# Performance work log

Hardware: AMD Instinct MI355X
Metric: run time of the kernel (lower is better)

The kernel has to match this reference:

```python
import jax, jax.numpy as jnp
import numpy as np

DIM = 4096
HEADS = 32
HEAD_DIM = 128
FFN_INNER = 4 * DIM  # GEGLU inner
EPS = 1e-6


def _mk(key, shape, scale=0.02):
    return jax.random.normal(key, shape, dtype=jnp.float32) * scale


def setup_inputs() -> dict:
    key = jax.random.key(0)
    ks = jax.random.split(key, 20)
    inp = {
        "video": jax.random.normal(ks[0], (1, 4096, DIM), dtype=jnp.float32),
        "text": jax.random.normal(ks[1], (1, 256, DIM), dtype=jnp.float32),
        # self-attention projections
        "wq": _mk(ks[2], (DIM, DIM)),
        "wk": _mk(ks[3], (DIM, DIM)),
        "wv": _mk(ks[4], (DIM, DIM)),
        "wo": _mk(ks[5], (DIM, DIM)),
        "q_norm_w": jnp.ones((DIM,), jnp.float32),
        "k_norm_w": jnp.ones((DIM,), jnp.float32),
        # cross-attention projections (q from video, k/v from text)
        "cwq": _mk(ks[6], (DIM, DIM)),
        "cwk": _mk(ks[7], (DIM, DIM)),
        "cwv": _mk(ks[8], (DIM, DIM)),
        "cwo": _mk(ks[9], (DIM, DIM)),
        "cq_norm_w": jnp.ones((DIM,), jnp.float32),
        "ck_norm_w": jnp.ones((DIM,), jnp.float32),
        # GEGLU FFN: proj -> (value, gate) -> value * gelu(gate) -> down
        "w_ff_proj": _mk(ks[10], (DIM, 2 * FFN_INNER)),
        "w_ff_down": _mk(ks[11], (FFN_INNER, DIM)),
    }
    return inp


def rmsnorm(x, w, eps=EPS):
    # RMSNorm over full hidden dim in fp32 (matches DistributedRMSNorm global math)
    x32 = x.astype(jnp.float32)
    rms = jax.lax.rsqrt(jnp.mean(x32 * x32, axis=-1, keepdims=True) + eps)
    return (x32 * rms) * w


def split_heads(x):  # [b,s,dim] -> [b,h,s,hd]
    b, s, _ = x.shape
    return x.reshape(b, s, HEADS, HEAD_DIM).transpose(0, 2, 1, 3)


def merge_heads(x):  # [b,h,s,hd] -> [b,s,dim]
    b, h, s, hd = x.shape
    return x.transpose(0, 2, 1, 3).reshape(b, s, h * hd)


def bmm_sdpa(q, k, v):
    # BMM + softmax fallback (explicit score matrix, as on Neuron)
    scale = 1.0 / np.sqrt(HEAD_DIM)
    scores = jnp.einsum("bhqd,bhkd->bhqk", q, k) * scale
    probs = jax.nn.softmax(scores, axis=-1)
    return jnp.einsum("bhqk,bhkd->bhqd", probs, v)


def attention(x_q, x_kv, wq, wk, wv, wo, qn, kn):
    q = rmsnorm(x_q @ wq, qn)
    k = rmsnorm(x_kv @ wk, kn)
    v = x_kv @ wv
    out = bmm_sdpa(split_heads(q), split_heads(k), split_heads(v))
    return merge_heads(out) @ wo


def geglu_ffn(x, w_proj, w_down):
    h = x @ w_proj
    val, gate = jnp.split(h, 2, axis=-1)
    return (val * jax.nn.gelu(gate)) @ w_down


def reference(video, text, wq, wk, wv, wo, q_norm_w, k_norm_w,
              cwq, cwk, cwv, cwo, cq_norm_w, ck_norm_w,
              w_ff_proj, w_ff_down):
    # video self-attention block slice
    h = video + attention(video, video, wq, wk, wv, wo, q_norm_w, k_norm_w)
    # text cross-attention
    h = h + attention(h, text, cwq, cwk, cwv, cwo, cq_norm_w, ck_norm_w)
    # GEGLU feed-forward
    h = h + geglu_ffn(h, w_ff_proj, w_ff_down)
    return h
```

## Files before the change

### kernel.cpp

```cpp
#include <hip/hip_runtime.h>
#include <cstdint>
#include <cstddef>

typedef __bf16 bf16;
typedef __bf16 bf16x8 __attribute__((ext_vector_type(8)));
typedef __bf16 bf16x4 __attribute__((ext_vector_type(4)));
typedef float f32x4 __attribute__((ext_vector_type(4)));

static constexpr int D = 4096;
static constexpr int S = 4096;
static constexpr int T = 256;
static constexpr int H = 32;
static constexpr int F = 16384;

__device__ __forceinline__ void gload16(const void* g, void* l) {
  __builtin_amdgcn_global_load_lds((const __attribute__((address_space(1))) void*)g,
                                   (__attribute__((address_space(3))) void*)l, 16, 0, 0);
}

#define MFMA16(a, b, c) __builtin_amdgcn_mfma_f32_16x16x32_bf16((a), (b), (c), 0, 0, 0)

__global__ __launch_bounds__(256) void k_cvt(const float* __restrict__ in, bf16* __restrict__ out, int n) {
  int i = (blockIdx.x * 256 + threadIdx.x) * 4;
  if (i >= n) return;
  float4 v = *(const float4*)(in + i);
  bf16x4 o = { (bf16)v.x, (bf16)v.y, (bf16)v.z, (bf16)v.w };
  *(bf16x4*)(out + i) = o;
}

__global__ __launch_bounds__(256) void k_tc(const float* __restrict__ in, bf16* __restrict__ out,
                                            int R, int C, int ldin) {
  __shared__ float tile[32][33];
  int c0 = blockIdx.x * 32, r0 = blockIdx.y * 32;
  int x = threadIdx.x, y = threadIdx.y;
  #pragma unroll
  for (int yy = y; yy < 32; yy += 8)
    tile[yy][x] = in[(size_t)(r0 + yy) * ldin + c0 + x];
  __syncthreads();
  #pragma unroll
  for (int yy = y; yy < 32; yy += 8)
    out[(size_t)(c0 + yy) * R + r0 + x] = (bf16)tile[x][yy];
}

__global__ __launch_bounds__(256) void k_tb(const bf16* __restrict__ in, bf16* __restrict__ out, int R, int C) {
  __shared__ bf16 tile[32][33];
  int c0 = blockIdx.x * 32, r0 = blockIdx.y * 32;
  int x = threadIdx.x, y = threadIdx.y;
  #pragma unroll
  for (int yy = y; yy < 32; yy += 8)
    tile[yy][x] = in[(size_t)(r0 + yy) * C + c0 + x];
  __syncthreads();
  #pragma unroll
  for (int yy = y; yy < 32; yy += 8)
    out[(size_t)(c0 + yy) * R + r0 + x] = tile[x][yy];
}

__global__ __launch_bounds__(256) void k_rms(const float* __restrict__ in, const float* __restrict__ w,
                                             bf16* __restrict__ out) {
  const int row = blockIdx.x, t = threadIdx.x;
  const float* x = in + (size_t)row * 4096;
  float4 v[4];
  float ss = 0.f;
  #pragma unroll
  for (int i = 0; i < 4; i++) {
    v[i] = *(const float4*)(x + t * 4 + i * 1024);
    ss += v[i].x * v[i].x + v[i].y * v[i].y + v[i].z * v[i].z + v[i].w * v[i].w;
  }
  #pragma unroll
  for (int off = 1; off < 64; off <<= 1) ss += __shfl_xor(ss, off, 64);
  __shared__ float red[4];
  if ((t & 63) == 0) red[t >> 6] = ss;
  __syncthreads();
  float rms = rsqrtf((red[0] + red[1] + red[2] + red[3]) * (1.f / 4096.f) + 1e-6f);
  #pragma unroll
  for (int i = 0; i < 4; i++) {
    const float4 wv = *(const float4*)(w + t * 4 + i * 1024);
    bf16x4 ov = { (bf16)(v[i].x * rms * wv.x), (bf16)(v[i].y * rms * wv.y),
                  (bf16)(v[i].z * rms * wv.z), (bf16)(v[i].w * rms * wv.w) };
    *(bf16x4*)(out + (size_t)row * 4096 + t * 4 + i * 1024) = ov;
  }
}

__device__ __forceinline__ void xcd_map(int orig, int XGM, int BYG, int BXG, int& by, int& bx) {
  const int xcd = orig & 7, oidx = orig >> 3;
  by = (xcd % XGM) * BYG + oidx % BYG;
  bx = (xcd / XGM) * BXG + oidx / BYG;
}

template <int MODE>
__global__ __launch_bounds__(512, 2) void k_gemm2(const bf16* __restrict__ A, const bf16* __restrict__ BT,
                                                  float* __restrict__ Cf, bf16* __restrict__ Cb,
                                                  const float* __restrict__ res,
                                                  int M, int N, int K, int XGM, int BYG, int BXG) {
  __shared__ bf16 LA[2][2][256 * 32];
  __shared__ bf16 LB[2][2][256 * 32];
  int by, bx;
  xcd_map(blockIdx.x, XGM, BYG, BXG, by, bx);
  const size_t m0 = (size_t)by * 256, n0 = (size_t)bx * 256;
  const int t = threadIdx.x;
  const int w = t >> 6, lane = t & 63;
  const int wm = w >> 2, wn = w & 3;
  const int g = lane >> 4, r15 = lane & 15;
  const int nt = K >> 6;
  const int sr0 = t >> 2, ss0 = t & 3;
  const int sr1 = (t + 512) >> 2, ss1 = (t + 512) & 3;
  const int sc0 = ((ss0 ^ ((sr0 >> 1) & 3)) << 3);
  const int sc1 = ((ss1 ^ ((sr1 >> 1) & 3)) << 3);
  f32x4 acc[8][4] = {};

  auto stA = [&](int db, int kh, int st) {
    const bf16* src = A + m0 * K + (size_t)st * 64 + kh * 32;
    gload16(src + (size_t)sr0 * K + sc0, &LA[db][kh][t * 8]);
    gload16(src + (size_t)sr1 * K + sc1, &LA[db][kh][(t + 512) * 8]);
  };
  auto stB = [&](int db, int kh, int st) {
    const bf16* src = BT + n0 * K + (size_t)st * 64 + kh * 32;
    gload16(src + (size_t)sr0 * K + sc0, &LB[db][kh][t * 8]);
    gload16(src + (size_t)sr1 * K + sc1, &LB[db][kh][(t + 512) * 8]);
  };

  stA(0, 0, 0); stB(0, 0, 0); stA(0, 1, 0); stB(0, 1, 0);
  stA(1, 0, 1); stB(1, 0, 1); stA(1, 1, 1);
  asm volatile("s_waitcnt vmcnt(6)" ::: "memory");
  __builtin_amdgcn_s_barrier();

  const int arow = wm * 128;

#define GEMM_TILE(DD, TC)                                                                     \
  {                                                                                           \
    const int t1 = ((TC) + 1 < nt) ? (TC) + 1 : nt - 1;                                       \
    const int t2 = ((TC) + 2 < nt) ? (TC) + 2 : nt - 1;                                       \
    bf16x8 af[8], b0, b1;                                                                     \
                                                                     \
    stB((DD) ^ 1, 1, t1);                                                                     \
    _Pragma("unroll")                                                                         \
    for (int mf = 0; mf < 8; ++mf) {                                                          \
      const int rr = arow + mf * 16 + r15;                                                    \
      af[mf] = *(const bf16x8*)&LA[DD][0][rr * 32 + ((g ^ ((rr >> 1) & 3)) << 3)];            \
    }                                                                                         \
    {                                                                                         \
      const int rb0 = wn * 64 + r15, rb1 = wn * 64 + 16 + r15;                                \
      b0 = *(const bf16x8*)&LB[DD][0][rb0 * 32 + ((g ^ ((rb0 >> 1) & 3)) << 3)];              \
      b1 = *(const bf16x8*)&LB[DD][0][rb1 * 32 + ((g ^ ((rb1 >> 1) & 3)) << 3)];              \
    }                                                                                         \
    __builtin_amdgcn_s_barrier();                                                             \
    __builtin_amdgcn_s_setprio(1);                                                            \
    _Pragma("unroll")                                                                         \
    for (int mf = 0; mf < 8; ++mf) {                                                          \
      acc[mf][0] = MFMA16(af[mf], b0, acc[mf][0]);                                            \
      acc[mf][1] = MFMA16(af[mf], b1, acc[mf][1]);                                            \
    }                                                                                         \
    __builtin_amdgcn_s_setprio(0);                                                            \
                                                                     \
    stA(DD, 0, t2);                                                                           \
    {                                                                                         \
      const int rb0 = wn * 64 + 32 + r15, rb1 = wn * 64 + 48 + r15;                           \
      b0 = *(const bf16x8*)&LB[DD][0][rb0 * 32 + ((g ^ ((rb0 >> 1) & 3)) << 3)];              \
      b1 = *(const bf16x8*)&LB[DD][0][rb1 * 32 + ((g ^ ((rb1 >> 1) & 3)) << 3)];              \
    }                                                                                         \
    __builtin_amdgcn_s_barrier();                                                             \
    __builtin_amdgcn_s_setprio(1);                                                            \
    _Pragma("unroll")                                                                         \
    for (int mf = 0; mf < 8; ++mf) {                                                          \
      acc[mf][2] = MFMA16(af[mf], b0, acc[mf][2]);                                            \
      acc[mf][3] = MFMA16(af[mf], b1, acc[mf][3]);                                            \
    }                                                                                         \
    __builtin_amdgcn_s_setprio(0);                                                            \
                                                                     \
    stB(DD, 0, t2);                                                                           \
    _Pragma("unroll")                                                                         \
    for (int mf = 0; mf < 8; ++mf) {                                                          \
      const int rr = arow + mf * 16 + r15;                                                    \
      af[mf] = *(const bf16x8*)&LA[DD][1][rr * 32 + ((g ^ ((rr >> 1) & 3)) << 3)];            \
    }                                                                                         \
    {                                                                                         \
      const int rb0 = wn * 64 + r15, rb1 = wn * 64 + 16 + r15;                                \
      b0 = *(const bf16x8*)&LB[DD][1][rb0 * 32 + ((g ^ ((rb0 >> 1) & 3)) << 3)];              \
      b1 = *(const bf16x8*)&LB[DD][1][rb1 * 32 + ((g ^ ((rb1 >> 1) & 3)) << 3)];              \
    }                                                                                         \
    __builtin_amdgcn_s_barrier();                                                             \
    __builtin_amdgcn_s_setprio(1);                                                            \
    _Pragma("unroll")                                                                         \
    for (int mf = 0; mf < 8; ++mf) {                                                          \
      acc[mf][0] = MFMA16(af[mf], b0, acc[mf][0]);                                            \
      acc[mf][1] = MFMA16(af[mf], b1, acc[mf][1]);                                            \
    }                                                                                         \
    __builtin_amdgcn_s_setprio(0);                                                            \
                                                                     \
    stA(DD, 1, t2);                                                                           \
    {                                                                                         \
      const int rb0 = wn * 64 + 32 + r15, rb1 = wn * 64 + 48 + r15;                           \
      b0 = *(const bf16x8*)&LB[DD][1][rb0 * 32 + ((g ^ ((rb0 >> 1) & 3)) << 3)];              \
      b1 = *(const bf16x8*)&LB[DD][1][rb1 * 32 + ((g ^ ((rb1 >> 1) & 3)) << 3)];              \
    }                                                                                         \
    asm volatile("s_waitcnt vmcnt(6)" ::: "memory");                                          \
    __builtin_amdgcn_s_barrier();                                                             \
    __builtin_amdgcn_s_setprio(1);                                                            \
    _Pragma("unroll")                                                                         \
    for (int mf = 0; mf < 8; ++mf) {                                                          \
      acc[mf][2] = MFMA16(af[mf], b0, acc[mf][2]);                                            \
      acc[mf][3] = MFMA16(af[mf], b1, acc[mf][3]);                                            \
    }                                                                                         \
    __builtin_amdgcn_s_setprio(0);                                                            \
  }

  for (int tt = 0; tt < nt; tt += 2) {
    GEMM_TILE(0, tt);
    GEMM_TILE(1, tt + 1);
  }
#undef GEMM_TILE

  #pragma unroll
  for (int mf = 0; mf < 8; ++mf)
    #pragma unroll
    for (int nf = 0; nf < 4; ++nf) {
      const size_t col = n0 + wn * 64 + nf * 16 + r15;
      #pragma unroll
      for (int rr = 0; rr < 4; ++rr) {
        const size_t row = m0 + wm * 128 + mf * 16 + g * 4 + rr;
        const size_t idx = row * (size_t)N + col;
        const float v = acc[mf][nf][rr];
        if (MODE == 0) Cf[idx] = v;
        else if (MODE == 1) Cb[idx] = (bf16)v;
        else Cf[idx] = v + res[idx];
      }
    }
}

__global__ __launch_bounds__(512, 2) void k_geglu2(const bf16* __restrict__ A, const bf16* __restrict__ BT,
                                                   bf16* __restrict__ G, int N, int K,
                                                   int XGM, int BYG, int BXG) {
  __shared__ bf16 LA[2][2][256 * 32];
  __shared__ bf16 LBv[2][2][128 * 32];
  __shared__ bf16 LBg[2][2][128 * 32];
  int by, bx;
  xcd_map(blockIdx.x, XGM, BYG, BXG, by, bx);
  const size_t m0 = (size_t)by * 256, n0 = (size_t)bx * 128;
  const int t = threadIdx.x;
  const int w = t >> 6, lane = t & 63;
  const int wm = w >> 2, wn = w & 3;
  const int g = lane >> 4, r15 = lane & 15;
  const int nt = K >> 6;
  const int sr0 = t >> 2, ss0 = t & 3;
  const int sr1 = (t + 512) >> 2, ss1 = (t + 512) & 3;
  const int sc0 = ((ss0 ^ ((sr0 >> 1) & 3)) << 3);
  const int sc1 = ((ss1 ^ ((sr1 >> 1) & 3)) << 3);
  f32x4 av[8][2] = {}, ag[8][2] = {};

  auto stA = [&](int db, int kh, int st) {
    const bf16* src = A + m0 * K + (size_t)st * 64 + kh * 32;
    gload16(src + (size_t)sr0 * K + sc0, &LA[db][kh][t * 8]);
    gload16(src + (size_t)sr1 * K + sc1, &LA[db][kh][(t + 512) * 8]);
  };
  auto stBv = [&](int db, int kh, int st) {
    const bf16* src = BT + n0 * K + (size_t)st * 64 + kh * 32;
    gload16(src + (size_t)sr0 * K + sc0, &LBv[db][kh][t * 8]);
  };
  auto stBg = [&](int db, int kh, int st) {
    const bf16* src = BT + ((size_t)N + n0) * K + (size_t)st * 64 + kh * 32;
    gload16(src + (size_t)sr0 * K + sc0, &LBg[db][kh][t * 8]);
  };

  stA(0, 0, 0); stBv(0, 0, 0); stBg(0, 0, 0); stA(0, 1, 0); stBv(0, 1, 0); stBg(0, 1, 0);
  stA(1, 0, 1); stBv(1, 0, 1); stBg(1, 0, 1); stA(1, 1, 1);
  asm volatile("s_waitcnt vmcnt(6)" ::: "memory");
  __builtin_amdgcn_s_barrier();

  const int arow = wm * 128;

#define GEGLU_TILE(DD, TC)                                                                    \
  {                                                                                           \
    const int t1 = ((TC) + 1 < nt) ? (TC) + 1 : nt - 1;                                       \
    const int t2 = ((TC) + 2 < nt) ? (TC) + 2 : nt - 1;                                       \
    bf16x8 af[8], b0, b1;                                                                     \
                                                                      \
    stBv((DD) ^ 1, 1, t1); stBg((DD) ^ 1, 1, t1);                                             \
    _Pragma("unroll")                                                                         \
    for (int mf = 0; mf < 8; ++mf) {                                                          \
      const int rr = arow + mf * 16 + r15;                                                    \
      af[mf] = *(const bf16x8*)&LA[DD][0][rr * 32 + ((g ^ ((rr >> 1) & 3)) << 3)];            \
    }                                                                                         \
    {                                                                                         \
      const int rb0 = wn * 32 + r15, rb1 = wn * 32 + 16 + r15;                                \
      b0 = *(const bf16x8*)&LBv[DD][0][rb0 * 32 + ((g ^ ((rb0 >> 1) & 3)) << 3)];             \
      b1 = *(const bf16x8*)&LBv[DD][0][rb1 * 32 + ((g ^ ((rb1 >> 1) & 3)) << 3)];             \
    }                                                                                         \
    __builtin_amdgcn_s_barrier();                                                             \
    __builtin_amdgcn_s_setprio(1);                                                            \
    _Pragma("unroll")                                                                         \
    for (int mf = 0; mf < 8; ++mf) {                                                          \
      av[mf][0] = MFMA16(af[mf], b0, av[mf][0]);                                              \
      av[mf][1] = MFMA16(af[mf], b1, av[mf][1]);                                              \
    }                                                                                         \
    __builtin_amdgcn_s_setprio(0);                                                            \
                                                                     \
    stA(DD, 0, t2);                                                                           \
    {                                                                                         \
      const int rb0 = wn * 32 + r15, rb1 = wn * 32 + 16 + r15;                                \
      b0 = *(const bf16x8*)&LBg[DD][0][rb0 * 32 + ((g ^ ((rb0 >> 1) & 3)) << 3)];             \
      b1 = *(const bf16x8*)&LBg[DD][0][rb1 * 32 + ((g ^ ((rb1 >> 1) & 3)) << 3)];             \
    }                                                                                         \
    __builtin_amdgcn_s_barrier();                                                             \
    __builtin_amdgcn_s_setprio(1);                                                            \
    _Pragma("unroll")                                                                         \
    for (int mf = 0; mf < 8; ++mf) {                                                          \
      ag[mf][0] = MFMA16(af[mf], b0, ag[mf][0]);                                              \
      ag[mf][1] = MFMA16(af[mf], b1, ag[mf][1]);                                              \
    }                                                                                         \
    __builtin_amdgcn_s_setprio(0);                                                            \
                                                                      \
    stBv(DD, 0, t2); stBg(DD, 0, t2);                                                         \
    _Pragma("unroll")                                                                         \
    for (int mf = 0; mf < 8; ++mf) {                                                          \
      const int rr = arow + mf * 16 + r15;                                                    \
      af[mf] = *(const bf16x8*)&LA[DD][1][rr * 32 + ((g ^ ((rr >> 1) & 3)) << 3)];            \
    }                                                                                         \
    {                                                                                         \
      const int rb0 = wn * 32 + r15, rb1 = wn * 32 + 16 + r15;                                \
      b0 = *(const bf16x8*)&LBv[DD][1][rb0 * 32 + ((g ^ ((rb0 >> 1) & 3)) << 3)];             \
      b1 = *(const bf16x8*)&LBv[DD][1][rb1 * 32 + ((g ^ ((rb1 >> 1) & 3)) << 3)];             \
    }                                                                                         \
    __builtin_amdgcn_s_barrier();                                                             \
    __builtin_amdgcn_s_setprio(1);                                                            \
    _Pragma("unroll")                                                                         \
    for (int mf = 0; mf < 8; ++mf) {                                                          \
      av[mf][0] = MFMA16(af[mf], b0, av[mf][0]);                                              \
      av[mf][1] = MFMA16(af[mf], b1, av[mf][1]);                                              \
    }                                                                                         \
    __builtin_amdgcn_s_setprio(0);                                                            \
                                                                     \
    stA(DD, 1, t2);                                                                           \
    {                                                                                         \
      const int rb0 = wn * 32 + r15, rb1 = wn * 32 + 16 + r15;                                \
      b0 = *(const bf16x8*)&LBg[DD][1][rb0 * 32 + ((g ^ ((rb0 >> 1) & 3)) << 3)];             \
      b1 = *(const bf16x8*)&LBg[DD][1][rb1 * 32 + ((g ^ ((rb1 >> 1) & 3)) << 3)];             \
    }                                                                                         \
    asm volatile("s_waitcnt vmcnt(6)" ::: "memory");                                          \
    __builtin_amdgcn_s_barrier();                                                             \
    __builtin_amdgcn_s_setprio(1);                                                            \
    _Pragma("unroll")                                                                         \
    for (int mf = 0; mf < 8; ++mf) {                                                          \
      ag[mf][0] = MFMA16(af[mf], b0, ag[mf][0]);                                              \
      ag[mf][1] = MFMA16(af[mf], b1, ag[mf][1]);                                              \
    }                                                                                         \
    __builtin_amdgcn_s_setprio(0);                                                            \
  }

  for (int tt = 0; tt < nt; tt += 2) {
    GEGLU_TILE(0, tt);
    GEGLU_TILE(1, tt + 1);
  }
#undef GEGLU_TILE

  #pragma unroll
  for (int mf = 0; mf < 8; ++mf)
    #pragma unroll
    for (int nf = 0; nf < 2; ++nf) {
      const size_t col = n0 + wn * 32 + nf * 16 + r15;
      #pragma unroll
      for (int rr = 0; rr < 4; ++rr) {
        const size_t row = m0 + wm * 128 + mf * 16 + g * 4 + rr;
        const float val = av[mf][nf][rr], gt = ag[mf][nf][rr];
        const float z = 1.595769122f * gt + 0.0713548162f * gt * gt * gt;
        const float gel = gt / (1.f + __expf(-z));
        G[row * (size_t)N + col] = (bf16)(val * gel);
      }
    }
}

template <int MODE>
__global__ __launch_bounds__(256) void k_gemm128(const bf16* __restrict__ A, const bf16* __restrict__ BT,
                                                 float* __restrict__ Cf, bf16* __restrict__ Cb,
                                                 int M, int N, int K) {
  __shared__ bf16 As[128 * 32];
  __shared__ bf16 Bs[128 * 32];
  const int t = threadIdx.x;
  const int lane = t & 63, w = t >> 6;
  const int wr = w >> 1, wc = w & 1;
  const int g = lane >> 4, r15 = lane & 15;
  const size_t m0 = (size_t)blockIdx.y * 128, n0 = (size_t)blockIdx.x * 128;
  f32x4 acc[4][4] = {};
  const int c0 = t, c1 = t + 256;
  const int ar0 = c0 >> 2, as0 = c0 & 3, ar1 = c1 >> 2, as1 = c1 & 3;
  const bf16* Ab = A + m0 * K;
  const bf16* Bb = BT + n0 * K;
  for (int k0 = 0; k0 < K; k0 += 32) {
    __syncthreads();
    gload16(Ab + (size_t)ar0 * K + k0 + ((as0 ^ (ar0 & 3)) << 3), &As[c0 * 8]);
    gload16(Ab + (size_t)ar1 * K + k0 + ((as1 ^ (ar1 & 3)) << 3), &As[c1 * 8]);
    gload16(Bb + (size_t)ar0 * K + k0 + ((as0 ^ (ar0 & 3)) << 3), &Bs[c0 * 8]);
    gload16(Bb + (size_t)ar1 * K + k0 + ((as1 ^ (ar1 & 3)) << 3), &Bs[c1 * 8]);
    __syncthreads();
    bf16x8 af[4], bfr[4];
    #pragma unroll
    for (int mi = 0; mi < 4; mi++) {
      int row = wr * 64 + mi * 16 + r15;
      af[mi] = *(const bf16x8*)&As[row * 32 + ((g ^ (row & 3)) << 3)];
    }
    #pragma unroll
    for (int ni = 0; ni < 4; ni++) {
      int row = wc * 64 + ni * 16 + r15;
      bfr[ni] = *(const bf16x8*)&Bs[row * 32 + ((g ^ (row & 3)) << 3)];
    }
    #pragma unroll
    for (int mi = 0; mi < 4; mi++)
      #pragma unroll
      for (int ni = 0; ni < 4; ni++)
        acc[mi][ni] = MFMA16(af[mi], bfr[ni], acc[mi][ni]);
  }
  #pragma unroll
  for (int mi = 0; mi < 4; mi++)
    #pragma unroll
    for (int ni = 0; ni < 4; ni++) {
      size_t col = n0 + wc * 64 + ni * 16 + r15;
      #pragma unroll
      for (int rr = 0; rr < 4; rr++) {
        size_t row = m0 + wr * 64 + mi * 16 + g * 4 + rr;
        size_t idx = row * (size_t)N + col;
        float v = acc[mi][ni][rr];
        if (MODE == 0) Cf[idx] = v;
        else Cb[idx] = (bf16)v;
      }
    }
}

__global__ __launch_bounds__(256) void k_attn(const bf16* __restrict__ Q, const bf16* __restrict__ Kb,
                                              const bf16* __restrict__ VT, bf16* __restrict__ O,
                                              int Skv) {
  __shared__ bf16 Kt[32 * 128];
  __shared__ bf16 Vt[128 * 32];
  __shared__ bf16 Pt[4][16 * 32];
  const int h = blockIdx.y;
  const int t = threadIdx.x, w = t >> 6, lane = t & 63;
  const int g = lane >> 4, r15 = lane & 15;
  const int q0 = blockIdx.x * 64 + w * 16;
  bf16x8 qf[4];
  #pragma unroll
  for (int c = 0; c < 4; c++)
    qf[c] = *(const bf16x8*)(Q + (size_t)(q0 + r15) * D + h * 128 + c * 32 + g * 8);
  f32x4 o[8] = {};
  float m_[4] = { -1e30f, -1e30f, -1e30f, -1e30f };
  float l_[4] = { 0.f, 0.f, 0.f, 0.f };
  const float scale = 0.08838834764831845f;
  for (int kt = 0; kt < Skv; kt += 32) {
    __syncthreads();
    #pragma unroll
    for (int cc = 0; cc < 2; cc++) {
      int c = t + cc * 256;
      int kr = c >> 4, ks = c & 15;
      gload16(Kb + (size_t)(kt + kr) * D + h * 128 + ((ks ^ (kr & 15)) << 3), &Kt[c * 8]);
      int vr = c >> 2, vs = c & 3;
      gload16(VT + (size_t)(h * 128 + vr) * Skv + kt + ((vs ^ (vr & 3)) << 3), &Vt[c * 8]);
    }
    __syncthreads();
    f32x4 s0 = {}, s1 = {};
    #pragma unroll
    for (int c = 0; c < 4; c++) {
      int row0 = r15, row1 = 16 + r15;
      bf16x8 kf0 = *(const bf16x8*)&Kt[row0 * 128 + (((4 * c + g) ^ (row0 & 15)) << 3)];
      bf16x8 kf1 = *(const bf16x8*)&Kt[row1 * 128 + (((4 * c + g) ^ (row1 & 15)) << 3)];
      s0 = MFMA16(qf[c], kf0, s0);
      s1 = MFMA16(qf[c], kf1, s1);
    }
    float al[4];
    #pragma unroll
    for (int rr = 0; rr < 4; rr++) {
      float v0 = s0[rr] * scale, v1 = s1[rr] * scale;
      float mx = fmaxf(v0, v1);
      #pragma unroll
      for (int off = 1; off < 16; off <<= 1) mx = fmaxf(mx, __shfl_xor(mx, off, 16));
      float mn = fmaxf(m_[rr], mx);
      al[rr] = __expf(m_[rr] - mn);
      float p0 = __expf(v0 - mn), p1 = __expf(v1 - mn);
      float sm = p0 + p1;
      #pragma unroll
      for (int off = 1; off < 16; off <<= 1) sm += __shfl_xor(sm, off, 16);
      l_[rr] = l_[rr] * al[rr] + sm;
      m_[rr] = mn;
      int prow = g * 4 + rr;
      int sl0 = r15 >> 3, sl1 = 2 + (r15 >> 3);
      Pt[w][prow * 32 + ((sl0 ^ (prow & 3)) << 3) + (r15 & 7)] = (bf16)p0;
      Pt[w][prow * 32 + ((sl1 ^ (prow & 3)) << 3) + (r15 & 7)] = (bf16)p1;
    }
    #pragma unroll
    for (int d = 0; d < 8; d++)
      #pragma unroll
      for (int rr = 0; rr < 4; rr++) o[d][rr] *= al[rr];
    bf16x8 pa = *(const bf16x8*)&Pt[w][r15 * 32 + ((g ^ (r15 & 3)) << 3)];
    #pragma unroll
    for (int d = 0; d < 8; d++) {
      int vrow = d * 16 + r15;
      bf16x8 vbf = *(const bf16x8*)&Vt[vrow * 32 + ((g ^ (vrow & 3)) << 3)];
      o[d] = MFMA16(pa, vbf, o[d]);
    }
  }
  #pragma unroll
  for (int rr = 0; rr < 4; rr++) {
    float inv = 1.f / l_[rr];
    #pragma unroll
    for (int d = 0; d < 8; d++)
      O[(size_t)(q0 + g * 4 + rr) * D + h * 128 + d * 16 + r15] = (bf16)(o[d][rr] * inv);
  }
}

extern "C" void kernel_launch(void* const* d_in, const int* in_sizes, int n_in,
                              void* d_out, int out_size, void* d_ws, size_t ws_size,
                              hipStream_t stream) {
  (void)in_sizes; (void)n_in; (void)out_size; (void)ws_size;
  const float* video = (const float*)d_in[0];
  const float* text  = (const float*)d_in[1];
  const float* wq    = (const float*)d_in[2];
  const float* wk    = (const float*)d_in[3];
  const float* wv    = (const float*)d_in[4];
  const float* wo    = (const float*)d_in[5];
  const float* qnw   = (const float*)d_in[6];
  const float* knw   = (const float*)d_in[7];
  const float* cwq   = (const float*)d_in[8];
  const float* cwk   = (const float*)d_in[9];
  const float* cwv   = (const float*)d_in[10];
  const float* cwo   = (const float*)d_in[11];
  const float* cqnw  = (const float*)d_in[12];
  const float* cknw  = (const float*)d_in[13];
  const float* ffp   = (const float*)d_in[14];
  const float* ffd   = (const float*)d_in[15];
  float* out = (float*)d_out;

  char* slab = (char*)d_ws;
  const size_t MB = 1024 * 1024;
  bf16*  wbuf  = (bf16*)slab;
  bf16*  vb    = (bf16*)(slab + 64 * MB);
  bf16*  vt    = (bf16*)(slab + 96 * MB);
  float* pre   = (float*)(slab + 128 * MB);
  bf16*  Hval  = (bf16*)(slab + 268 * MB);
  char* p = slab + 402 * MB;
  auto take = [&](size_t bytes) { char* r = p; p += (bytes + 255) & ~(size_t)255; return r; };
  bf16* xb   = (bf16*)take((size_t)S * D * 2);
  bf16* qb   = (bf16*)take((size_t)S * D * 2);
  bf16* kb   = (bf16*)take((size_t)S * D * 2);
  bf16* ab   = (bf16*)take((size_t)S * D * 2);
  float* h1  = (float*)take((size_t)S * D * 4);
  bf16* tbuf = (bf16*)take((size_t)T * D * 2);
  bf16* ckb  = (bf16*)take((size_t)T * D * 2);
  bf16* cvb  = (bf16*)take((size_t)T * D * 2);
  bf16* cvt_ = (bf16*)take((size_t)T * D * 2);
  float* h2  = out;

  dim3 b256(256), b512(512), btc(32, 8);
  const int GRID_DD = 256, GRID_GG = 2048;

  k_cvt<<<(S * D) / 1024, b256, 0, stream>>>(video, xb, S * D);
  k_tc<<<dim3(D / 32, D / 32), btc, 0, stream>>>(wq, wbuf, D, D, D);
  k_gemm2<0><<<GRID_DD, b512, 0, stream>>>(xb, wbuf, pre, nullptr, nullptr, S, D, D, 2, 8, 4);
  k_rms<<<S, b256, 0, stream>>>(pre, qnw, qb);
  k_tc<<<dim3(D / 32, D / 32), btc, 0, stream>>>(wk, wbuf, D, D, D);
  k_gemm2<0><<<GRID_DD, b512, 0, stream>>>(xb, wbuf, pre, nullptr, nullptr, S, D, D, 2, 8, 4);
  k_rms<<<S, b256, 0, stream>>>(pre, knw, kb);
  k_tc<<<dim3(D / 32, D / 32), btc, 0, stream>>>(wv, wbuf, D, D, D);
  k_gemm2<1><<<GRID_DD, b512, 0, stream>>>(xb, wbuf, nullptr, vb, nullptr, S, D, D, 2, 8, 4);
  k_tb<<<dim3(D / 32, S / 32), btc, 0, stream>>>(vb, vt, S, D);
  k_attn<<<dim3(S / 64, H), b256, 0, stream>>>(qb, kb, vt, ab, S);
  k_tc<<<dim3(D / 32, D / 32), btc, 0, stream>>>(wo, wbuf, D, D, D);
  k_gemm2<2><<<GRID_DD, b512, 0, stream>>>(ab, wbuf, h1, nullptr, video, S, D, D, 2, 8, 4);

  k_cvt<<<(S * D) / 1024, b256, 0, stream>>>(h1, xb, S * D);
  k_tc<<<dim3(D / 32, D / 32), btc, 0, stream>>>(cwq, wbuf, D, D, D);
  k_gemm2<0><<<GRID_DD, b512, 0, stream>>>(xb, wbuf, pre, nullptr, nullptr, S, D, D, 2, 8, 4);
  k_rms<<<S, b256, 0, stream>>>(pre, cqnw, qb);
  k_cvt<<<(T * D) / 1024, b256, 0, stream>>>(text, tbuf, T * D);
  k_tc<<<dim3(D / 32, D / 32), btc, 0, stream>>>(cwk, wbuf, D, D, D);
  k_gemm128<0><<<dim3(D / 128, T / 128), b256, 0, stream>>>(tbuf, wbuf, pre, nullptr, T, D, D);
  k_rms<<<T, b256, 0, stream>>>(pre, cknw, ckb);
  k_tc<<<dim3(D / 32, D / 32), btc, 0, stream>>>(cwv, wbuf, D, D, D);
  k_gemm128<1><<<dim3(D / 128, T / 128), b256, 0, stream>>>(tbuf, wbuf, nullptr, cvb, T, D, D);
  k_tb<<<dim3(D / 32, T / 32), btc, 0, stream>>>(cvb, cvt_, T, D);
  k_attn<<<dim3(S / 64, H), b256, 0, stream>>>(qb, ckb, cvt_, ab, T);
  k_tc<<<dim3(D / 32, D / 32), btc, 0, stream>>>(cwo, wbuf, D, D, D);
  k_gemm2<2><<<GRID_DD, b512, 0, stream>>>(ab, wbuf, h2, nullptr, h1, S, D, D, 2, 8, 4);

  k_cvt<<<(S * D) / 1024, b256, 0, stream>>>(h2, xb, S * D);
  k_tc<<<dim3((2 * F) / 32, D / 32), btc, 0, stream>>>(ffp, wbuf, D, 2 * F, 2 * F);
  k_geglu2<<<GRID_GG, b512, 0, stream>>>(xb, wbuf, Hval, F, D, 2, 8, 32);
  k_tc<<<dim3(D / 32, F / 32), btc, 0, stream>>>(ffd, wbuf, F, D, D);
  k_gemm2<2><<<GRID_DD, b512, 0, stream>>>(Hval, wbuf, out, nullptr, h2, S, D, F, 2, 8, 4);
}
```

Before: 4.051 ms.

## Store pre-norm projections in bf16, fuse residual bf16 cast, relax GEMM waitcnts

Q/K projection GEMMs now write bf16 instead of fp32 pre-norm outputs, and k_rms reads bf16, which halves that intermediate traffic. The residual-output GEMMs gain a mode that also writes a bf16 copy, so the separate fp32-to-bf16 conversion kernels before the next stage go away. GEMM and GEGLU pipelines raise the vmcnt wait threshold and add a wait before the first-half barrier, changing how many loads stay in flight. Rounding pre-norm values to bf16 before RMSNorm adds some precision loss.

```diff
diff --git a/kernel.cpp b/kernel.cpp
--- a/kernel.cpp
+++ b/kernel.cpp
@@ -55,16 +55,17 @@
     out[(size_t)(c0 + yy) * R + r0 + x] = tile[x][yy];
 }
 
-__global__ __launch_bounds__(256) void k_rms(const float* __restrict__ in, const float* __restrict__ w,
+__global__ __launch_bounds__(256) void k_rms(const bf16* __restrict__ in, const float* __restrict__ w,
                                              bf16* __restrict__ out) {
   const int row = blockIdx.x, t = threadIdx.x;
-  const float* x = in + (size_t)row * 4096;
-  float4 v[4];
+  const bf16* x = in + (size_t)row * 4096;
+  float xv[16];
   float ss = 0.f;
   #pragma unroll
-  for (int i = 0; i < 4; i++) {
-    v[i] = *(const float4*)(x + t * 4 + i * 1024);
-    ss += v[i].x * v[i].x + v[i].y * v[i].y + v[i].z * v[i].z + v[i].w * v[i].w;
+  for (int i = 0; i < 2; i++) {
+    bf16x8 b = *(const bf16x8*)(x + t * 8 + i * 2048);
+    #pragma unroll
+    for (int j = 0; j < 8; j++) { xv[i * 8 + j] = (float)b[j]; ss += xv[i * 8 + j] * xv[i * 8 + j]; }
   }
   #pragma unroll
   for (int off = 1; off < 64; off <<= 1) ss += __shfl_xor(ss, off, 64);
@@ -73,11 +74,15 @@
   __syncthreads();
   float rms = rsqrtf((red[0] + red[1] + red[2] + red[3]) * (1.f / 4096.f) + 1e-6f);
   #pragma unroll
-  for (int i = 0; i < 4; i++) {
-    const float4 wv = *(const float4*)(w + t * 4 + i * 1024);
-    bf16x4 ov = { (bf16)(v[i].x * rms * wv.x), (bf16)(v[i].y * rms * wv.y),
-                  (bf16)(v[i].z * rms * wv.z), (bf16)(v[i].w * rms * wv.w) };
-    *(bf16x4*)(out + (size_t)row * 4096 + t * 4 + i * 1024) = ov;
+  for (int i = 0; i < 2; i++) {
+    float4 w0 = *(const float4*)(w + t * 8 + i * 2048);
+    float4 w1 = *(const float4*)(w + t * 8 + i * 2048 + 4);
+    bf16x8 ov;
+    ov[0] = (bf16)(xv[i * 8 + 0] * rms * w0.x); ov[1] = (bf16)(xv[i * 8 + 1] * rms * w0.y);
+    ov[2] = (bf16)(xv[i * 8 + 2] * rms * w0.z); ov[3] = (bf16)(xv[i * 8 + 3] * rms * w0.w);
+    ov[4] = (bf16)(xv[i * 8 + 4] * rms * w1.x); ov[5] = (bf16)(xv[i * 8 + 5] * rms * w1.y);
+    ov[6] = (bf16)(xv[i * 8 + 6] * rms * w1.z); ov[7] = (bf16)(xv[i * 8 + 7] * rms * w1.w);
+    *(bf16x8*)(out + (size_t)row * 4096 + t * 8 + i * 2048) = ov;
   }
 }
 
@@ -121,7 +126,7 @@
 
   stA(0, 0, 0); stB(0, 0, 0); stA(0, 1, 0); stB(0, 1, 0);
   stA(1, 0, 1); stB(1, 0, 1); stA(1, 1, 1);
-  asm volatile("s_waitcnt vmcnt(6)" ::: "memory");
+  asm volatile("s_waitcnt vmcnt(10)" ::: "memory");
   __builtin_amdgcn_s_barrier();
 
   const int arow = wm * 128;
@@ -158,6 +163,7 @@
       b0 = *(const bf16x8*)&LB[DD][0][rb0 * 32 + ((g ^ ((rb0 >> 1) & 3)) << 3)];              \
       b1 = *(const bf16x8*)&LB[DD][0][rb1 * 32 + ((g ^ ((rb1 >> 1) & 3)) << 3)];              \
     }                                                                                         \
+    asm volatile("s_waitcnt vmcnt(10)" ::: "memory");                                         \
     __builtin_amdgcn_s_barrier();                                                             \
     __builtin_amdgcn_s_setprio(1);                                                            \
     _Pragma("unroll")                                                                         \
@@ -193,7 +199,7 @@
       b0 = *(const bf16x8*)&LB[DD][1][rb0 * 32 + ((g ^ ((rb0 >> 1) & 3)) << 3)];              \
       b1 = *(const bf16x8*)&LB[DD][1][rb1 * 32 + ((g ^ ((rb1 >> 1) & 3)) << 3)];              \
     }                                                                                         \
-    asm volatile("s_waitcnt vmcnt(6)" ::: "memory");                                          \
+    asm volatile("s_waitcnt vmcnt(10)" ::: "memory");                                         \
     __builtin_amdgcn_s_barrier();                                                             \
     __builtin_amdgcn_s_setprio(1);                                                            \
     _Pragma("unroll")                                                                         \
@@ -222,7 +228,8 @@
         const float v = acc[mf][nf][rr];
         if (MODE == 0) Cf[idx] = v;
         else if (MODE == 1) Cb[idx] = (bf16)v;
-        else Cf[idx] = v + res[idx];
+        else if (MODE == 2) Cf[idx] = v + res[idx];
+        else { const float s = v + res[idx]; Cf[idx] = s; Cb[idx] = (bf16)s; }
       }
     }
 }
@@ -263,7 +270,7 @@
 
   stA(0, 0, 0); stBv(0, 0, 0); stBg(0, 0, 0); stA(0, 1, 0); stBv(0, 1, 0); stBg(0, 1, 0);
   stA(1, 0, 1); stBv(1, 0, 1); stBg(1, 0, 1); stA(1, 1, 1);
-  asm volatile("s_waitcnt vmcnt(6)" ::: "memory");
+  asm volatile("s_waitcnt vmcnt(10)" ::: "memory");
   __builtin_amdgcn_s_barrier();
 
   const int arow = wm * 128;
@@ -300,6 +307,7 @@
       b0 = *(const bf16x8*)&LBg[DD][0][rb0 * 32 + ((g ^ ((rb0 >> 1) & 3)) << 3)];             \
       b1 = *(const bf16x8*)&LBg[DD][0][rb1 * 32 + ((g ^ ((rb1 >> 1) & 3)) << 3)];             \
     }                                                                                         \
+    asm volatile("s_waitcnt vmcnt(10)" ::: "memory");                                         \
     __builtin_amdgcn_s_barrier();                                                             \
     __builtin_amdgcn_s_setprio(1);                                                            \
     _Pragma("unroll")                                                                         \
@@ -335,7 +343,7 @@
       b0 = *(const bf16x8*)&LBg[DD][1][rb0 * 32 + ((g ^ ((rb0 >> 1) & 3)) << 3)];             \
       b1 = *(const bf16x8*)&LBg[DD][1][rb1 * 32 + ((g ^ ((rb1 >> 1) & 3)) << 3)];             \
     }                                                                                         \
-    asm volatile("s_waitcnt vmcnt(6)" ::: "memory");                                          \
+    asm volatile("s_waitcnt vmcnt(10)" ::: "memory");                                         \
     __builtin_amdgcn_s_barrier();                                                             \
     __builtin_amdgcn_s_setprio(1);                                                            \
     _Pragma("unroll")                                                                         \
@@ -530,7 +538,7 @@
   bf16*  wbuf  = (bf16*)slab;
   bf16*  vb    = (bf16*)(slab + 64 * MB);
   bf16*  vt    = (bf16*)(slab + 96 * MB);
-  float* pre   = (float*)(slab + 128 * MB);
+  bf16*  preb  = (bf16*)(slab + 128 * MB);
   bf16*  Hval  = (bf16*)(slab + 268 * MB);
   char* p = slab + 402 * MB;
   auto take = [&](size_t bytes) { char* r = p; p += (bytes + 255) & ~(size_t)255; return r; };
@@ -550,34 +558,32 @@
 
   k_cvt<<<(S * D) / 1024, b256, 0, stream>>>(video, xb, S * D);
   k_tc<<<dim3(D / 32, D / 32), btc, 0, stream>>>(wq, wbuf, D, D, D);
-  k_gemm2<0><<<GRID_DD, b512, 0, stream>>>(xb, wbuf, pre, nullptr, nullptr, S, D, D, 2, 8, 4);
-  k_rms<<<S, b256, 0, stream>>>(pre, qnw, qb);
+  k_gemm2<1><<<GRID_DD, b512, 0, stream>>>(xb, wbuf, nullptr, preb, nullptr, S, D, D, 2, 8, 4);
+  k_rms<<<S, b256, 0, stream>>>(preb, qnw, qb);
   k_tc<<<dim3(D / 32, D / 32), btc, 0, stream>>>(wk, wbuf, D, D, D);
-  k_gemm2<0><<<GRID_DD, b512, 0, stream>>>(xb, wbuf, pre, nullptr, nullptr, S, D, D, 2, 8, 4);
-  k_rms<<<S, b256, 0, stream>>>(pre, knw, kb);
+  k_gemm2<1><<<GRID_DD, b512, 0, stream>>>(xb, wbuf, nullptr, preb, nullptr, S, D, D, 2, 8, 4);
+  k_rms<<<S, b256, 0, stream>>>(preb, knw, kb);
   k_tc<<<dim3(D / 32, D / 32), btc, 0, stream>>>(wv, wbuf, D, D, D);
   k_gemm2<1><<<GRID_DD, b512, 0, stream>>>(xb, wbuf, nullptr, vb, nullptr, S, D, D, 2, 8, 4);
   k_tb<<<dim3(D / 32, S / 32), btc, 0, stream>>>(vb, vt, S, D);
   k_attn<<<dim3(S / 64, H), b256, 0, stream>>>(qb, kb, vt, ab, S);
   k_tc<<<dim3(D / 32, D / 32), btc, 0, stream>>>(wo, wbuf, D, D, D);
-  k_gemm2<2><<<GRID_DD, b512, 0, stream>>>(ab, wbuf, h1, nullptr, video, S, D, D, 2, 8, 4);
-
-  k_cvt<<<(S * D) / 1024, b256, 0, stream>>>(h1, xb, S * D);
+  k_gemm2<3><<<GRID_DD, b512, 0, stream>>>(ab, wbuf, h1, xb, video, S, D, D, 2, 8, 4);
+
   k_tc<<<dim3(D / 32, D / 32), btc, 0, stream>>>(cwq, wbuf, D, D, D);
-  k_gemm2<0><<<GRID_DD, b512, 0, stream>>>(xb, wbuf, pre, nullptr, nullptr, S, D, D, 2, 8, 4);
-  k_rms<<<S, b256, 0, stream>>>(pre, cqnw, qb);
+  k_gemm2<1><<<GRID_DD, b512, 0, stream>>>(xb, wbuf, nullptr, preb, nullptr, S, D, D, 2, 8, 4);
+  k_rms<<<S, b256, 0, stream>>>(preb, cqnw, qb);
   k_cvt<<<(T * D) / 1024, b256, 0, stream>>>(text, tbuf, T * D);
   k_tc<<<dim3(D / 32, D / 32), btc, 0, stream>>>(cwk, wbuf, D, D, D);
-  k_gemm128<0><<<dim3(D / 128, T / 128), b256, 0, stream>>>(tbuf, wbuf, pre, nullptr, T, D, D);
-  k_rms<<<T, b256, 0, stream>>>(pre, cknw, ckb);
+  k_gemm128<1><<<dim3(D / 128, T / 128), b256, 0, stream>>>(tbuf, wbuf, nullptr, preb, T, D, D);
+  k_rms<<<T, b256, 0, stream>>>(preb, cknw, ckb);
   k_tc<<<dim3(D / 32, D / 32), btc, 0, stream>>>(cwv, wbuf, D, D, D);
   k_gemm128<1><<<dim3(D / 128, T / 128), b256, 0, stream>>>(tbuf, wbuf, nullptr, cvb, T, D, D);
   k_tb<<<dim3(D / 32, T / 32), btc, 0, stream>>>(cvb, cvt_, T, D);
   k_attn<<<dim3(S / 64, H), b256, 0, stream>>>(qb, ckb, cvt_, ab, T);
   k_tc<<<dim3(D / 32, D / 32), btc, 0, stream>>>(cwo, wbuf, D, D, D);
-  k_gemm2<2><<<GRID_DD, b512, 0, stream>>>(ab, wbuf, h2, nullptr, h1, S, D, D, 2, 8, 4);
-
-  k_cvt<<<(S * D) / 1024, b256, 0, stream>>>(h2, xb, S * D);
+  k_gemm2<3><<<GRID_DD, b512, 0, stream>>>(ab, wbuf, h2, xb, h1, S, D, D, 2, 8, 4);
+
   k_tc<<<dim3((2 * F) / 32, D / 32), btc, 0, stream>>>(ffp, wbuf, D, 2 * F, 2 * F);
   k_geglu2<<<GRID_GG, b512, 0, stream>>>(xb, wbuf, Hval, F, D, 2, 8, 32);
   k_tc<<<dim3(D / 32, F / 32), btc, 0, stream>>>(ffd, wbuf, F, D, D);
```

After: 4.024 ms. About the same (-0.7%).
